# Kernel tuning notes

Measured on AMD Instinct MI355X. Metric: run time of the kernel, lower is better.

## Reference

```python
import jax, jax.numpy as jnp
import numpy as np

H = 12          # num_heads
T = 8           # num_temp_tokens (frames per video clip)


def _conv1d(z, w, b):
    # z: (Bv, C, T), w: (C_out, C_in, 3), padding=1, stride=1 (matches nn.Conv1d)
    y = jax.lax.conv_general_dilated(z, w, window_strides=(1,), padding=[(1, 1)],
                                     dimension_numbers=('NCH', 'OIH', 'NCH'))
    return y + b[None, :, None]


def setup_inputs() -> dict:
    key = jax.random.key(0)
    ks = jax.random.split(key, 9)
    B, N, C = 64, 197, 768
    s = 0.02
    return {
        'x': jax.random.normal(ks[0], (B, N, C), jnp.float32),
        'w_qkv': jax.random.normal(ks[1], (3 * C, C), jnp.float32) * s,
        'b_qkv': jax.random.normal(ks[2], (3 * C,), jnp.float32) * s,
        'w_proj': jax.random.normal(ks[3], (C, C), jnp.float32) * s,
        'b_proj': jax.random.normal(ks[4], (C,), jnp.float32) * s,
        'conv_q_w': jax.random.normal(ks[5], (C, C, 3), jnp.float32) * s,
        'conv_q_b': jax.random.normal(ks[6], (C,), jnp.float32) * s,
        'conv_k_w': jax.random.normal(ks[7], (C, C, 3), jnp.float32) * s,
        'conv_k_b': jax.random.normal(ks[8], (C,), jnp.float32) * s,
    }


def reference(x, w_qkv, b_qkv, w_proj, b_proj, conv_q_w, conv_q_b, conv_k_w, conv_k_b):
    B, N, C = x.shape
    Dh = C // H
    scale = Dh ** -0.5

    # temporal context from the CLS token across frames of each clip
    g = x[:, 0, :].reshape(B // T, T, C).transpose(0, 2, 1)          # (Bv, C, T)
    tcq = _conv1d(g, conv_q_w, conv_q_b).transpose(0, 2, 1).reshape(B, H, 1, Dh)
    tck = _conv1d(g, conv_k_w, conv_k_b).transpose(0, 2, 1).reshape(B, H, 1, Dh)

    qkv = (x @ w_qkv.T + b_qkv).reshape(B, N, 3, H, Dh).transpose(2, 0, 3, 1, 4)
    q, k, v = qkv[0], qkv[1], qkv[2]                                  # (B, H, N, Dh)

    # bias-added attention: (q + tcq) (k + tck)^T
    scores = jnp.einsum('bhnd,bhmd->bhnm', q + tcq, k + tck) * scale  # (B, H, N, N)
    attn = jax.nn.softmax(scores, axis=-1)
    out = jnp.einsum('bhnm,bhmd->bhnd', attn, v)                      # (B, H, N, Dh)
    out = out.transpose(0, 2, 1, 3).reshape(B, N, C)
    return out @ w_proj.T + b_proj
```

## Files before the change

### kernel.cpp

```cpp
#include <hip/hip_runtime.h>
#include <hip/hip_bf16.h>
#include <stdint.h>

typedef __attribute__((ext_vector_type(8))) short s16x8;
typedef __attribute__((ext_vector_type(4))) float f32x4;

#define MFMA16(a, b, c) __builtin_amdgcn_mfma_f32_16x16x32_bf16((a), (b), (c), 0, 0, 0)
#define SBAR() __builtin_amdgcn_s_barrier()

__device__ __forceinline__ void gl_lds16(const void* g, void* l) {
  __builtin_amdgcn_global_load_lds(
      (__attribute__((address_space(1))) void*)(void*)g,
      (__attribute__((address_space(3))) void*)l,
      16, 0, 0);
}

__device__ __forceinline__ unsigned short f2bf(float f) {
  union { float f; uint32_t u; } c; c.f = f;
  return (unsigned short)((c.u + 0x7FFFu + ((c.u >> 16) & 1u)) >> 16);
}

__device__ __forceinline__ f32x4 max4(f32x4 a, f32x4 b) {
  f32x4 c;
  c[0] = fmaxf(a[0], b[0]); c[1] = fmaxf(a[1], b[1]);
  c[2] = fmaxf(a[2], b[2]); c[3] = fmaxf(a[3], b[3]);
  return c;
}

__device__ __forceinline__ void xcd_swz(int GX, int GY, int& bx, int& by) {
  int nwg = GX * GY;
  int lid = by * GX + bx;
  int q = nwg >> 3, rm = nwg & 7;
  int xcd = lid & 7, off = lid >> 3;
  int nid = (xcd < rm ? xcd * (q + 1) : rm * (q + 1) + (xcd - rm) * q) + off;
  bx = nid % GX;
  by = nid / GX;
}

__global__ __launch_bounds__(256) void cvt_conv(
    const float* __restrict__ x, unsigned short* __restrict__ x_bf, int na4,
    const float* __restrict__ wqkv, unsigned short* __restrict__ wqkv_bf, int nb4,
    const float* __restrict__ wproj, unsigned short* __restrict__ wproj_bf, int nc4,
    const float* __restrict__ cqw, const float* __restrict__ cqb,
    const float* __restrict__ ckw, const float* __restrict__ ckb,
    float* __restrict__ tcq, float* __restrict__ tck) {
  const int tid = threadIdx.x;
  const int bid = blockIdx.x;
  if (bid < 192) {
    __shared__ float g[768][10];
    const int clip = bid / 24;
    const int chunk = bid % 24;
    for (int i = tid; i < 768 * 8; i += 256) {
      int tt = i / 768, ci = i % 768;
      g[ci][tt + 1] = x[(size_t)(clip * 8 + tt) * 151296 + ci];
    }
    for (int i = tid; i < 768; i += 256) { g[i][0] = 0.f; g[i][9] = 0.f; }
    __syncthreads();
    const int co = chunk * 32 + (tid >> 3);
    const int t = tid & 7;
    float aq = 0.f, ak = 0.f;
    const float* wqp = cqw + (size_t)co * 2304;
    const float* wkp = ckw + (size_t)co * 2304;
    for (int ci = 0; ci < 768; ++ci) {
      float g0 = g[ci][t], g1 = g[ci][t + 1], g2 = g[ci][t + 2];
      aq += g0 * wqp[ci * 3 + 0] + g1 * wqp[ci * 3 + 1] + g2 * wqp[ci * 3 + 2];
      ak += g0 * wkp[ci * 3 + 0] + g1 * wkp[ci * 3 + 1] + g2 * wkp[ci * 3 + 2];
    }
    int b = clip * 8 + t;
    tcq[b * 768 + co] = aq + cqb[co];
    tck[b * 768 + co] = ak + ckb[co];
    return;
  }
  int i = (bid - 192) * 256 + tid;
  const float* src; unsigned short* dst; int j;
  if (i < na4) { src = x; dst = x_bf; j = i; }
  else if (i < na4 + nb4) { src = wqkv; dst = wqkv_bf; j = i - na4; }
  else if (i < na4 + nb4 + nc4) { src = wproj; dst = wproj_bf; j = i - na4 - nb4; }
  else return;
  float4 v = ((const float4*)src)[j];
  ushort4 o;
  o.x = f2bf(v.x); o.y = f2bf(v.y); o.z = f2bf(v.z); o.w = f2bf(v.w);
  ((ushort4*)dst)[j] = o;
}

__global__ __launch_bounds__(1024, 4) void qkv_attn(
    const unsigned short* __restrict__ X,
    const unsigned short* __restrict__ Wq,
    const float* __restrict__ bias,
    const float* __restrict__ tcq, const float* __restrict__ tck,
    unsigned short* __restrict__ O) {
  union __align__(16) Smem {
    struct {
      unsigned short Xs[3][208][64];
      unsigned short Ws[3][192][64];
    } st;
    struct {
      unsigned short Qs[208][72];
      unsigned short Ks[208][72];
      unsigned short VTs[64][232];
      unsigned short Ps[13][16][40];
    } at;
  };
  __shared__ Smem U;
  __shared__ float tcb[3][64];

  const int tid = threadIdx.x;
  const int w = tid >> 6, lane = tid & 63;
  int bx = blockIdx.x, by0 = 0;
  xcd_swz(gridDim.x, 1, bx, by0);
  const int b = bx / 12, h = bx % 12;

  if (tid < 192) {
    int sec = tid >> 6, d = tid & 63;
    float v = bias[sec * 768 + h * 64 + d];
    if (sec == 0) v += tcq[b * 768 + h * 64 + d];
    else if (sec == 1) v += tck[b * 768 + h * 64 + d];
    tcb[sec][d] = v;
  }

  const int wm = w >> 2, wn = w & 3;
  const int r = lane & 15, gq = lane >> 4;
  const int lrow = lane >> 3;
  const int lsw = ((lane & 7) ^ (lrow & 7)) * 8;
  const int mfn = (wm == 3) ? 4 : 3;

  f32x4 acc[4][3] = {};
  const size_t xbase = (size_t)b * 197 * 768;

  const int swzk[2] = { ((0 + gq) ^ (r & 7)) * 16, ((4 + gq) ^ (r & 7)) * 16 };
  const int rowA = (wm * 48 + r) * 128;
  const int rowB = (wn * 48 + r) * 128;

  auto stage = [&](int buf, int kc) {
#pragma unroll
    for (int j = 0; j < 2; ++j) {
      int c = w + j * 16;
      if (c < 26) {
        int row = c * 8 + lrow;
        gl_lds16(X + xbase + (size_t)row * 768 + kc * 64 + lsw,
                 (char*)&U.st.Xs[buf][0][0] + c * 1024);
      }
    }
#pragma unroll
    for (int j = 0; j < 2; ++j) {
      int c = w + j * 16;
      if (c < 24) {
        int wrow = c * 8 + lrow;
        int sec = wrow >> 6;
        gl_lds16(Wq + (size_t)(sec * 768 + h * 64 + (wrow & 63)) * 768 + kc * 64 + lsw,
                 (char*)&U.st.Ws[buf][0][0] + c * 1024);
      }
    }
  };

#define WAIT_OWN()                                                 \
  do {                                                             \
    if (w < 8)       asm volatile("s_waitcnt vmcnt(4)" ::: "memory"); \
    else if (w < 10) asm volatile("s_waitcnt vmcnt(3)" ::: "memory"); \
    else             asm volatile("s_waitcnt vmcnt(2)" ::: "memory"); \
  } while (0)

  stage(0, 0);
  stage(1, 1);
  WAIT_OWN();
  SBAR();

#pragma unroll
  for (int kc = 0; kc < 12; ++kc) {
    if (kc + 2 < 12) stage((kc + 2) % 3, kc + 2);
    const char* xb = (const char*)&U.st.Xs[kc % 3][0][0] + rowA;
    const char* wb = (const char*)&U.st.Ws[kc % 3][0][0] + rowB;
    __builtin_amdgcn_s_setprio(1);
#pragma unroll
    for (int kk = 0; kk < 2; ++kk) {
      s16x8 bfrg[3];
#pragma unroll
      for (int nf = 0; nf < 3; ++nf)
        bfrg[nf] = *(const s16x8*)(wb + nf * 2048 + swzk[kk]);
#pragma unroll
      for (int mf = 0; mf < 4; ++mf) {
        if (mf < mfn) {
          s16x8 afr = *(const s16x8*)(xb + mf * 2048 + swzk[kk]);
#pragma unroll
          for (int nf = 0; nf < 3; ++nf) acc[mf][nf] = MFMA16(afr, bfrg[nf], acc[mf][nf]);
        }
      }
    }
    __builtin_amdgcn_s_setprio(0);
    if (kc < 10) {
      WAIT_OWN();
      SBAR();
    } else if (kc == 10) {
      asm volatile("s_waitcnt vmcnt(0)" ::: "memory");
      SBAR();
    }
  }
  __syncthreads();

  for (int i = tid; i < 64 * 35; i += 1024) {
    int d = i / 35, c = 197 + i % 35;
    U.at.VTs[d][c] = 0;
  }
#pragma unroll
  for (int mf = 0; mf < 4; ++mf) {
    if (mf < mfn) {
#pragma unroll
      for (int nf = 0; nf < 3; ++nf) {
        int ncol = wn * 48 + nf * 16 + r;
        int sec = ncol >> 6, d = ncol & 63;
        float bb = tcb[sec][d];
#pragma unroll
        for (int rr = 0; rr < 4; ++rr) {
          int mrow = wm * 48 + mf * 16 + gq * 4 + rr;
          unsigned short bv = f2bf(acc[mf][nf][rr] + bb);
          if (sec == 0)      U.at.Qs[mrow][d] = bv;
          else if (sec == 1) U.at.Ks[mrow][d] = bv;
          else if (mrow < 197) U.at.VTs[d][mrow] = bv;
        }
      }
    }
  }
  __syncthreads();

  const int g = gq;
  for (int qt = w; qt < 13; qt += 16) {
    const int q0 = qt * 16;
    int qrow = q0 + r; if (qrow > 196) qrow = 196;
    s16x8 aq0 = *(const s16x8*)&U.at.Qs[qrow][g * 8];
    s16x8 aq1 = *(const s16x8*)&U.at.Qs[qrow][32 + g * 8];

    f32x4 s[13];
    __builtin_amdgcn_s_setprio(1);
#pragma unroll
    for (int j = 0; j < 13; ++j) {
      f32x4 z = {};
      z = MFMA16(aq0, *(const s16x8*)&U.at.Ks[j * 16 + r][g * 8], z);
      z = MFMA16(aq1, *(const s16x8*)&U.at.Ks[j * 16 + r][32 + g * 8], z);
      s[j] = z;
    }
    __builtin_amdgcn_s_setprio(0);
    if (r >= 5) { s[12][0] = -1e30f; s[12][1] = -1e30f; s[12][2] = -1e30f; s[12][3] = -1e30f; }

    f32x4 mx = s[0];
#pragma unroll
    for (int j = 1; j < 13; ++j) mx = max4(mx, s[j]);
#pragma unroll
    for (int off = 1; off < 16; off <<= 1) {
      f32x4 o_;
      o_[0] = __shfl_xor(mx[0], off, 64); o_[1] = __shfl_xor(mx[1], off, 64);
      o_[2] = __shfl_xor(mx[2], off, 64); o_[3] = __shfl_xor(mx[3], off, 64);
      mx = max4(mx, o_);
    }
    const float cexp = 0.125f * 1.44269504088896f;
    f32x4 sum = {};
#pragma unroll
    for (int j = 0; j < 13; ++j) {
      f32x4 p;
      p[0] = exp2f((s[j][0] - mx[0]) * cexp); p[1] = exp2f((s[j][1] - mx[1]) * cexp);
      p[2] = exp2f((s[j][2] - mx[2]) * cexp); p[3] = exp2f((s[j][3] - mx[3]) * cexp);
      s[j] = p;
      sum += p;
    }
#pragma unroll
    for (int off = 1; off < 16; off <<= 1) {
      sum[0] += __shfl_xor(sum[0], off, 64); sum[1] += __shfl_xor(sum[1], off, 64);
      sum[2] += __shfl_xor(sum[2], off, 64); sum[3] += __shfl_xor(sum[3], off, 64);
    }

    f32x4 o4[4] = {};
    for (int ks = 0; ks < 7; ++ks) {
      int j0 = ks * 2;
#pragma unroll
      for (int jj = 0; jj < 2; ++jj) {
        int jt = j0 + jj;
        int colb = jj * 16 + r;
        if (jt < 13) {
          f32x4 p = s[jt < 13 ? jt : 0];
          U.at.Ps[w][g * 4 + 0][colb] = f2bf(p[0]);
          U.at.Ps[w][g * 4 + 1][colb] = f2bf(p[1]);
          U.at.Ps[w][g * 4 + 2][colb] = f2bf(p[2]);
          U.at.Ps[w][g * 4 + 3][colb] = f2bf(p[3]);
        } else {
          U.at.Ps[w][g * 4 + 0][colb] = 0; U.at.Ps[w][g * 4 + 1][colb] = 0;
          U.at.Ps[w][g * 4 + 2][colb] = 0; U.at.Ps[w][g * 4 + 3][colb] = 0;
        }
      }
      asm volatile("s_waitcnt lgkmcnt(0)" ::: "memory");
      s16x8 ap = *(const s16x8*)&U.at.Ps[w][r][g * 8];
      __builtin_amdgcn_s_setprio(1);
#pragma unroll
      for (int n = 0; n < 4; ++n)
        o4[n] = MFMA16(ap, *(const s16x8*)&U.at.VTs[n * 16 + r][ks * 32 + g * 8], o4[n]);
      __builtin_amdgcn_s_setprio(0);
    }

    f32x4 rinv;
    rinv[0] = 1.0f / sum[0]; rinv[1] = 1.0f / sum[1];
    rinv[2] = 1.0f / sum[2]; rinv[3] = 1.0f / sum[3];
#pragma unroll
    for (int n = 0; n < 4; ++n) {
#pragma unroll
      for (int rr = 0; rr < 4; ++rr) {
        int qr = q0 + g * 4 + rr;
        if (qr < 197)
          O[((size_t)(b * 197 + qr)) * 768 + h * 64 + n * 16 + r] = f2bf(o4[n][rr] * rinv[rr]);
      }
    }
  }
#undef WAIT_OWN
}

__global__ __launch_bounds__(512, 4) void proj_gemm(
    const unsigned short* __restrict__ A,
    const unsigned short* __restrict__ Bw,
    const float* __restrict__ bias,
    float* __restrict__ Out) {
  __shared__ __align__(16) unsigned short As[2][192][64];
  __shared__ __align__(16) unsigned short Bs[2][128][64];
  const int tid = threadIdx.x;
  const int w = tid >> 6, lane = tid & 63;
  const int wm = w >> 1, wn = w & 1;
  const int r = lane & 15, gq = lane >> 4;
  int bx = blockIdx.x, by = blockIdx.y;
  xcd_swz(gridDim.x, gridDim.y, bx, by);
  const int m0 = by * 192, n0 = bx * 128;
  const int lrow = lane >> 3;
  const int lsw = ((lane & 7) ^ (lrow & 7)) * 8;

  f32x4 acc[3][4] = {};

  auto stage = [&](int buf, int kt) {
#pragma unroll
    for (int j = 0; j < 3; ++j) {
      int c = w + j * 8;
      int row = c * 8 + lrow;
      gl_lds16(A + (size_t)(m0 + row) * 768 + kt * 64 + lsw, (char*)&As[buf][0][0] + c * 1024);
    }
#pragma unroll
    for (int j = 0; j < 2; ++j) {
      int c = w + j * 8;
      int row = c * 8 + lrow;
      gl_lds16(Bw + (size_t)(n0 + row) * 768 + kt * 64 + lsw, (char*)&Bs[buf][0][0] + c * 1024);
    }
  };

  stage(0, 0);
  stage(1, 1);
  asm volatile("s_waitcnt vmcnt(5)" ::: "memory");
  SBAR();

#pragma unroll
  for (int kt = 0; kt < 12; ++kt) {
    const int cur = kt & 1;
    s16x8 af[2][3], bfr[2][4];
#pragma unroll
    for (int kk = 0; kk < 2; ++kk) {
#pragma unroll
      for (int m = 0; m < 3; ++m) {
        int row = wm * 48 + m * 16 + r;
        af[kk][m] = *(const s16x8*)((const char*)&As[cur][0][0] + row * 128 +
                                    (((kk * 4 + gq) ^ (r & 7)) * 16));
      }
#pragma unroll
      for (int n = 0; n < 4; ++n) {
        int row = wn * 64 + n * 16 + r;
        bfr[kk][n] = *(const s16x8*)((const char*)&Bs[cur][0][0] + row * 128 +
                                     (((kk * 4 + gq) ^ (r & 7)) * 16));
      }
    }
    asm volatile("s_waitcnt lgkmcnt(0)" ::: "memory");
    __builtin_amdgcn_sched_barrier(0);
    SBAR();
    if (kt + 2 < 12) stage(cur, kt + 2);
    __builtin_amdgcn_s_setprio(1);
#pragma unroll
    for (int kk = 0; kk < 2; ++kk)
#pragma unroll
      for (int m = 0; m < 3; ++m)
#pragma unroll
        for (int n = 0; n < 4; ++n) acc[m][n] = MFMA16(af[kk][m], bfr[kk][n], acc[m][n]);
    __builtin_amdgcn_s_setprio(0);
    if (kt < 11) {
      if (kt < 10) asm volatile("s_waitcnt vmcnt(5)" ::: "memory");
      else         asm volatile("s_waitcnt vmcnt(0)" ::: "memory");
      SBAR();
    }
  }

#pragma unroll
  for (int m = 0; m < 3; ++m) {
#pragma unroll
    for (int n = 0; n < 4; ++n) {
#pragma unroll
      for (int rr = 0; rr < 4; ++rr) {
        int M = m0 + wm * 48 + m * 16 + gq * 4 + rr;
        int N = n0 + wn * 64 + n * 16 + r;
        if (M < 12608) Out[(size_t)M * 768 + N] = acc[m][n][rr] + bias[N];
      }
    }
  }
}

extern "C" void kernel_launch(void* const* d_in, const int* in_sizes, int n_in,
                              void* d_out, int out_size, void* d_ws, size_t ws_size,
                              hipStream_t stream) {
  const float* x       = (const float*)d_in[0];
  const float* w_qkv   = (const float*)d_in[1];
  const float* b_qkv   = (const float*)d_in[2];
  const float* w_proj  = (const float*)d_in[3];
  const float* b_proj  = (const float*)d_in[4];
  const float* conv_qw = (const float*)d_in[5];
  const float* conv_qb = (const float*)d_in[6];
  const float* conv_kw = (const float*)d_in[7];
  const float* conv_kb = (const float*)d_in[8];
  float* out = (float*)d_out;

  char* ws = (char*)d_ws;
  size_t off = 0;
  auto alloc = [&](size_t n) {
    char* p = ws + off;
    off = (off + n + 255) & ~(size_t)255;
    return p;
  };
  unsigned short* x_bf    = (unsigned short*)alloc(12608ull * 768 * 2);
  unsigned short* ao_bf   = (unsigned short*)alloc(12608ull * 768 * 2);
  unsigned short* wqkv_bf = (unsigned short*)alloc(2304ull * 768 * 2);
  unsigned short* wproj_bf= (unsigned short*)alloc(768ull * 768 * 2);
  float* tcq = (float*)alloc(64 * 768 * 4);
  float* tck = (float*)alloc(64 * 768 * 4);
  if (off > ws_size) return;

  const int na4 = 2420736, nb4 = 442368, nc4 = 147456;
  const int cvt_blocks = (na4 + nb4 + nc4 + 255) / 256;
  cvt_conv<<<dim3(192 + cvt_blocks), 256, 0, stream>>>(
      x, x_bf, na4, w_qkv, wqkv_bf, nb4, w_proj, wproj_bf, nc4,
      conv_qw, conv_qb, conv_kw, conv_kb, tcq, tck);
  qkv_attn<<<dim3(768), 1024, 0, stream>>>(x_bf, wqkv_bf, b_qkv, tcq, tck, ao_bf);
  proj_gemm<<<dim3(6, 66), 512, 0, stream>>>(ao_bf, wproj_bf, b_proj, out);
}
```

Before: 170.9 us.

## Split temporal conv over input channels and retile proj GEMM per batch

The temporal conv1d work is split four ways over input channels. This gives 768 blocks instead of 192, and each block writes partial sums that qkv_attn adds back together while it loads the bias. The conv biases are folded into the qkv bias by a separate small kernel. The projection GEMM is restructured to use 1024-thread blocks, one per batch and 192-column slice, with a 3-stage buffer and no padded rows spanning batches. This mirrors the qkv_attn tiling. The cost is an extra kernel launch, partial-sum traffic, and a bias_comb allocation placed after the workspace size check.

New measurement: 152.7 us. 10.6% less time.

```diff
diff --git a/kernel.cpp b/kernel.cpp
--- a/kernel.cpp
+++ b/kernel.cpp
@@ -41,37 +41,39 @@
     const float* __restrict__ x, unsigned short* __restrict__ x_bf, int na4,
     const float* __restrict__ wqkv, unsigned short* __restrict__ wqkv_bf, int nb4,
     const float* __restrict__ wproj, unsigned short* __restrict__ wproj_bf, int nc4,
-    const float* __restrict__ cqw, const float* __restrict__ cqb,
-    const float* __restrict__ ckw, const float* __restrict__ ckb,
-    float* __restrict__ tcq, float* __restrict__ tck) {
+    const float* __restrict__ cqw, const float* __restrict__ ckw,
+    float* __restrict__ tcpq, float* __restrict__ tcpk) {
   const int tid = threadIdx.x;
   const int bid = blockIdx.x;
-  if (bid < 192) {
-    __shared__ float g[768][10];
-    const int clip = bid / 24;
-    const int chunk = bid % 24;
-    for (int i = tid; i < 768 * 8; i += 256) {
-      int tt = i / 768, ci = i % 768;
-      g[ci][tt + 1] = x[(size_t)(clip * 8 + tt) * 151296 + ci];
-    }
-    for (int i = tid; i < 768; i += 256) { g[i][0] = 0.f; g[i][9] = 0.f; }
+  if (bid < 768) {
+    __shared__ float g[192][10];
+    const int clip = bid / 96;
+    const int rem = bid % 96;
+    const int chunk = rem >> 2;
+    const int part = rem & 3;
+    const int ci0 = part * 192;
+    for (int i = tid; i < 192 * 8; i += 256) {
+      int tt = i / 192, ci = i % 192;
+      g[ci][tt + 1] = x[(size_t)(clip * 8 + tt) * 151296 + ci0 + ci];
+    }
+    for (int i = tid; i < 192; i += 256) { g[i][0] = 0.f; g[i][9] = 0.f; }
     __syncthreads();
     const int co = chunk * 32 + (tid >> 3);
     const int t = tid & 7;
     float aq = 0.f, ak = 0.f;
-    const float* wqp = cqw + (size_t)co * 2304;
-    const float* wkp = ckw + (size_t)co * 2304;
-    for (int ci = 0; ci < 768; ++ci) {
+    const float* wqp = cqw + (size_t)co * 2304 + ci0 * 3;
+    const float* wkp = ckw + (size_t)co * 2304 + ci0 * 3;
+    for (int ci = 0; ci < 192; ++ci) {
       float g0 = g[ci][t], g1 = g[ci][t + 1], g2 = g[ci][t + 2];
       aq += g0 * wqp[ci * 3 + 0] + g1 * wqp[ci * 3 + 1] + g2 * wqp[ci * 3 + 2];
       ak += g0 * wkp[ci * 3 + 0] + g1 * wkp[ci * 3 + 1] + g2 * wkp[ci * 3 + 2];
     }
     int b = clip * 8 + t;
-    tcq[b * 768 + co] = aq + cqb[co];
-    tck[b * 768 + co] = ak + ckb[co];
+    tcpq[part * 49152 + b * 768 + co] = aq;
+    tcpk[part * 49152 + b * 768 + co] = ak;
     return;
   }
-  int i = (bid - 192) * 256 + tid;
+  int i = (bid - 768) * 256 + tid;
   const float* src; unsigned short* dst; int j;
   if (i < na4) { src = x; dst = x_bf; j = i; }
   else if (i < na4 + nb4) { src = wqkv; dst = wqkv_bf; j = i - na4; }
@@ -87,7 +89,7 @@
     const unsigned short* __restrict__ X,
     const unsigned short* __restrict__ Wq,
     const float* __restrict__ bias,
-    const float* __restrict__ tcq, const float* __restrict__ tck,
+    const float* __restrict__ tcpq, const float* __restrict__ tcpk,
     unsigned short* __restrict__ O) {
   union __align__(16) Smem {
     struct {
@@ -113,8 +115,12 @@
   if (tid < 192) {
     int sec = tid >> 6, d = tid & 63;
     float v = bias[sec * 768 + h * 64 + d];
-    if (sec == 0) v += tcq[b * 768 + h * 64 + d];
-    else if (sec == 1) v += tck[b * 768 + h * 64 + d];
+    if (sec < 2) {
+      const float* tp = (sec == 0) ? tcpq : tcpk;
+      int idx = b * 768 + h * 64 + d;
+#pragma unroll
+      for (int p = 0; p < 4; ++p) v += tp[p * 49152 + idx];
+    }
     tcb[sec][d] = v;
   }
 
@@ -310,95 +316,111 @@
 #undef WAIT_OWN
 }
 
-__global__ __launch_bounds__(512, 4) void proj_gemm(
+__global__ __launch_bounds__(1024, 4) void proj_gemm(
     const unsigned short* __restrict__ A,
     const unsigned short* __restrict__ Bw,
     const float* __restrict__ bias,
     float* __restrict__ Out) {
-  __shared__ __align__(16) unsigned short As[2][192][64];
-  __shared__ __align__(16) unsigned short Bs[2][128][64];
+  __shared__ __align__(16) unsigned short Xs[3][208][64];
+  __shared__ __align__(16) unsigned short Ws[3][192][64];
   const int tid = threadIdx.x;
   const int w = tid >> 6, lane = tid & 63;
-  const int wm = w >> 1, wn = w & 1;
+  int bx = blockIdx.x, by0 = 0;
+  xcd_swz(gridDim.x, 1, bx, by0);
+  const int b = bx >> 2, nt = bx & 3;
+  const int wm = w >> 2, wn = w & 3;
   const int r = lane & 15, gq = lane >> 4;
-  int bx = blockIdx.x, by = blockIdx.y;
-  xcd_swz(gridDim.x, gridDim.y, bx, by);
-  const int m0 = by * 192, n0 = bx * 128;
   const int lrow = lane >> 3;
   const int lsw = ((lane & 7) ^ (lrow & 7)) * 8;
-
-  f32x4 acc[3][4] = {};
-
-  auto stage = [&](int buf, int kt) {
-#pragma unroll
-    for (int j = 0; j < 3; ++j) {
-      int c = w + j * 8;
-      int row = c * 8 + lrow;
-      gl_lds16(A + (size_t)(m0 + row) * 768 + kt * 64 + lsw, (char*)&As[buf][0][0] + c * 1024);
-    }
+  const int mfn = (wm == 3) ? 4 : 3;
+
+  f32x4 acc[4][3] = {};
+  const size_t abase = (size_t)b * 197 * 768;
+  const int swzk[2] = { ((0 + gq) ^ (r & 7)) * 16, ((4 + gq) ^ (r & 7)) * 16 };
+  const int rowA = (wm * 48 + r) * 128;
+  const int rowB = (wn * 48 + r) * 128;
+
+  auto stage = [&](int buf, int kc) {
 #pragma unroll
     for (int j = 0; j < 2; ++j) {
-      int c = w + j * 8;
-      int row = c * 8 + lrow;
-      gl_lds16(Bw + (size_t)(n0 + row) * 768 + kt * 64 + lsw, (char*)&Bs[buf][0][0] + c * 1024);
+      int c = w + j * 16;
+      if (c < 26) {
+        int row = c * 8 + lrow;
+        gl_lds16(A + abase + (size_t)row * 768 + kc * 64 + lsw,
+                 (char*)&Xs[buf][0][0] + c * 1024);
+      }
+    }
+#pragma unroll
+    for (int j = 0; j < 2; ++j) {
+      int c = w + j * 16;
+      if (c < 24) {
+        int wrow = c * 8 + lrow;
+        gl_lds16(Bw + (size_t)(nt * 192 + wrow) * 768 + kc * 64 + lsw,
+                 (char*)&Ws[buf][0][0] + c * 1024);
+      }
     }
   };
+
+#define WAIT_OWN()                                                 \
+  do {                                                             \
+    if (w < 8)       asm volatile("s_waitcnt vmcnt(4)" ::: "memory"); \
+    else if (w < 10) asm volatile("s_waitcnt vmcnt(3)" ::: "memory"); \
+    else             asm volatile("s_waitcnt vmcnt(2)" ::: "memory"); \
+  } while (0)
 
   stage(0, 0);
   stage(1, 1);
-  asm volatile("s_waitcnt vmcnt(5)" ::: "memory");
+  WAIT_OWN();
   SBAR();
 
 #pragma unroll
-  for (int kt = 0; kt < 12; ++kt) {
-    const int cur = kt & 1;
-    s16x8 af[2][3], bfr[2][4];
+  for (int kc = 0; kc < 12; ++kc) {
+    if (kc + 2 < 12) stage((kc + 2) % 3, kc + 2);
+    const char* xb = (const char*)&Xs[kc % 3][0][0] + rowA;
+    const char* wb = (const char*)&Ws[kc % 3][0][0] + rowB;
+    __builtin_amdgcn_s_setprio(1);
 #pragma unroll
     for (int kk = 0; kk < 2; ++kk) {
-#pragma unroll
-      for (int m = 0; m < 3; ++m) {
-        int row = wm * 48 + m * 16 + r;
-        af[kk][m] = *(const s16x8*)((const char*)&As[cur][0][0] + row * 128 +
-                                    (((kk * 4 + gq) ^ (r & 7)) * 16));
-      }
-#pragma unroll
-      for (int n = 0; n < 4; ++n) {
-        int row = wn * 64 + n * 16 + r;
-        bfr[kk][n] = *(const s16x8*)((const char*)&Bs[cur][0][0] + row * 128 +
-                                     (((kk * 4 + gq) ^ (r & 7)) * 16));
-      }
-    }
-    asm volatile("s_waitcnt lgkmcnt(0)" ::: "memory");
-    __builtin_amdgcn_sched_barrier(0);
-    SBAR();
-    if (kt + 2 < 12) stage(cur, kt + 2);
-    __builtin_amdgcn_s_setprio(1);
-#pragma unroll
-    for (int kk = 0; kk < 2; ++kk)
-#pragma unroll
-      for (int m = 0; m < 3; ++m)
-#pragma unroll
-        for (int n = 0; n < 4; ++n) acc[m][n] = MFMA16(af[kk][m], bfr[kk][n], acc[m][n]);
+      s16x8 bfrg[3];
+#pragma unroll
+      for (int nf = 0; nf < 3; ++nf)
+        bfrg[nf] = *(const s16x8*)(wb + nf * 2048 + swzk[kk]);
+#pragma unroll
+      for (int mf = 0; mf < 4; ++mf) {
+        if (mf < mfn) {
+          s16x8 afr = *(const s16x8*)(xb + mf * 2048 + swzk[kk]);
+#pragma unroll
+          for (int nf = 0; nf < 3; ++nf) acc[mf][nf] = MFMA16(afr, bfrg[nf], acc[mf][nf]);
+        }
+      }
+    }
     __builtin_amdgcn_s_setprio(0);
-    if (kt < 11) {
-      if (kt < 10) asm volatile("s_waitcnt vmcnt(5)" ::: "memory");
-      else         asm volatile("s_waitcnt vmcnt(0)" ::: "memory");
+    if (kc < 10) {
+      WAIT_OWN();
       SBAR();
-    }
-  }
-
-#pragma unroll
-  for (int m = 0; m < 3; ++m) {
-#pragma unroll
-    for (int n = 0; n < 4; ++n) {
-#pragma unroll
-      for (int rr = 0; rr < 4; ++rr) {
-        int M = m0 + wm * 48 + m * 16 + gq * 4 + rr;
-        int N = n0 + wn * 64 + n * 16 + r;
-        if (M < 12608) Out[(size_t)M * 768 + N] = acc[m][n][rr] + bias[N];
-      }
-    }
-  }
+    } else if (kc == 10) {
+      asm volatile("s_waitcnt vmcnt(0)" ::: "memory");
+      SBAR();
+    }
+  }
+
+#pragma unroll
+  for (int mf = 0; mf < 4; ++mf) {
+    if (mf < mfn) {
+#pragma unroll
+      for (int nf = 0; nf < 3; ++nf) {
+        int N = nt * 192 + wn * 48 + nf * 16 + r;
+        float bb = bias[N];
+#pragma unroll
+        for (int rr = 0; rr < 4; ++rr) {
+          int mrow = wm * 48 + mf * 16 + gq * 4 + rr;
+          if (mrow < 197)
+            Out[((size_t)(b * 197 + mrow)) * 768 + N] = acc[mf][nf][rr] + bb;
+        }
+      }
+    }
+  }
+#undef WAIT_OWN
 }
 
 extern "C" void kernel_launch(void* const* d_in, const int* in_sizes, int n_in,
@@ -426,15 +448,33 @@
   unsigned short* ao_bf   = (unsigned short*)alloc(12608ull * 768 * 2);
   unsigned short* wqkv_bf = (unsigned short*)alloc(2304ull * 768 * 2);
   unsigned short* wproj_bf= (unsigned short*)alloc(768ull * 768 * 2);
-  float* tcq = (float*)alloc(64 * 768 * 4);
-  float* tck = (float*)alloc(64 * 768 * 4);
+  float* tcpq = (float*)alloc(4ull * 64 * 768 * 4);
+  float* tcpk = (float*)alloc(4ull * 64 * 768 * 4);
   if (off > ws_size) return;
+
+  float* bias_comb = (float*)alloc(2304ull * 4);
+  {
+  }
 
   const int na4 = 2420736, nb4 = 442368, nc4 = 147456;
   const int cvt_blocks = (na4 + nb4 + nc4 + 255) / 256;
-  cvt_conv<<<dim3(192 + cvt_blocks), 256, 0, stream>>>(
+  cvt_conv<<<dim3(768 + cvt_blocks), 256, 0, stream>>>(
       x, x_bf, na4, w_qkv, wqkv_bf, nb4, w_proj, wproj_bf, nc4,
-      conv_qw, conv_qb, conv_kw, conv_kb, tcq, tck);
-  qkv_attn<<<dim3(768), 1024, 0, stream>>>(x_bf, wqkv_bf, b_qkv, tcq, tck, ao_bf);
-  proj_gemm<<<dim3(6, 66), 512, 0, stream>>>(ao_bf, wproj_bf, b_proj, out);
-}
+      conv_qw, conv_kw, tcpq, tcpk);
+  {
+    struct L {
+      static __global__ void k(const float* bq, const float* cq, const float* ck,
+                               float* o) {
+        int i = blockIdx.x * 256 + threadIdx.x;
+        if (i >= 2304) return;
+        float v = bq[i];
+        if (i < 768) v += cq[i];
+        else if (i < 1536) v += ck[i - 768];
+        o[i] = v;
+      }
+    };
+    L::k<<<dim3(9), 256, 0, stream>>>(b_qkv, conv_qb, conv_kb, bias_comb);
+  }
+  qkv_attn<<<dim3(768), 1024, 0, stream>>>(x_bf, wqkv_bf, bias_comb, tcpq, tcpk, ao_bf);
+  proj_gemm<<<dim3(256), 1024, 0, stream>>>(ao_bf, wproj_bf, b_proj, out);
+}
```
